# Kernel optimization log

Measured on AMD Instinct MI355X. Metric: run time of the kernel, lower is better.

The kernel has to match this reference:

```python
import jax, jax.numpy as jnp
import numpy as np

HID = 768
NUM_HEADS = 12
HEAD_DIM = HID // NUM_HEADS
MASK_VALUE = -1.0e9
EPS = 1.0e-4  # module's self.eps, also used as the diagonal fill constant


def setup_inputs() -> dict:
    key = jax.random.key(0)
    k1, k2, k3 = jax.random.split(key, 3)
    B, M = 16, 512
    ocr_features = jax.random.normal(k1, (B, M, HID), dtype=jnp.float32)
    # prior neighbor-attention from previous layer, probabilities in [0,1)
    prior = jax.random.uniform(k2, (B, 1, M, M), dtype=jnp.float32)
    Wq = jax.random.normal(k3, (HID, HID), dtype=jnp.float32) / np.sqrt(HID)
    bq = jnp.zeros((HID,), dtype=jnp.float32)
    ocr_features_mask = jnp.ones((B, M), dtype=jnp.int32)
    return {"ocr_features": ocr_features, "prior": prior, "Wq": Wq, "bq": bq,
            "ocr_features_mask": ocr_features_mask}


def reference(ocr_features, prior, Wq, bq, ocr_features_mask):
    B, M, _ = ocr_features.shape
    # Module uses q_linear for Q, K (and V, which is unused) -> Q == K.
    q = (ocr_features @ Wq + bq).reshape(B, M, NUM_HEADS, HEAD_DIM)
    q = q.transpose(0, 2, 1, 3)  # (B, H, M, D)
    # note: scaled by head_dim (not sqrt), as in the source
    scores = jnp.einsum('bhid,bhjd->bhij', q, q) / HEAD_DIM  # (B, H, M, M)

    dt = scores.dtype
    prev_word_mask = jnp.eye(M, k=1, dtype=dt)   # superdiagonal
    next_word_mask = jnp.eye(M, k=-1, dtype=dt)  # subdiagonal
    main_diag_mask = jnp.eye(M, dtype=dt)

    # neighbor mask: only prev/next word positions that are valid OCR tokens
    neibor_mask = ((prev_word_mask + next_word_mask)[None, :, :] > 0) & \
                  (ocr_features_mask[:, None, :] > 0)  # (B, M, M)
    scores = jnp.where(neibor_mask[:, None, :, :], scores, MASK_VALUE)
    neibor_attn = jax.nn.softmax(scores, axis=-1)
    # symmetrize: sqrt(a * a^T + eps)
    neibor_attn = jnp.sqrt(neibor_attn * jnp.swapaxes(neibor_attn, -1, -2) + EPS)
    neibor_attn = prior + (1.0 - prior) * neibor_attn

    # log-space cumulative product via triangular matmuls
    tri = jnp.triu(jnp.ones((M, M), dtype=dt))  # (M, M), incl. diagonal
    # keep only superdiagonal log-probs, cumulative-sum to the right via tri
    t = jnp.where(prev_word_mask > 0, jnp.log(neibor_attn + 1e-9), 0.0) @ tri
    g_attn = jnp.exp(jnp.einsum('ij,bhjk->bhik', tri, t))
    # zero out diagonal and lower triangle (tri - diag == 0 there)
    g_attn = jnp.where((tri - main_diag_mask) > 0, g_attn, 0.0)
    g_attn = g_attn + jnp.swapaxes(g_attn, -1, -2) + \
             jnp.where(main_diag_mask > 0, neibor_attn, EPS)
    return (g_attn, neibor_attn)
```

## Files before the change

### kernel.cpp

```cpp
#include <hip/hip_runtime.h>
#include <cstdint>
#include <cstddef>

#define B_   16
#define M_   512
#define HID_ 768
#define NH_  12
#define HD_  64

typedef short s16x8 __attribute__((ext_vector_type(8)));
typedef float f32x4 __attribute__((ext_vector_type(4)));
typedef unsigned short u16x8 __attribute__((ext_vector_type(8)));
typedef unsigned short u16x4 __attribute__((ext_vector_type(4)));

__device__ __forceinline__ unsigned short f2bf(float f) {
    unsigned int u = __builtin_bit_cast(unsigned int, f);
    u = u + 0x7FFFu + ((u >> 16) & 1u);
    return (unsigned short)(u >> 16);
}

__device__ __forceinline__ void gld_lds16(const void* g, void* lds) {
    __builtin_amdgcn_global_load_lds(
        (const __attribute__((address_space(1))) unsigned int*)g,
        (__attribute__((address_space(3))) unsigned int*)lds,
        16, 0, 0);
}

__launch_bounds__(256)
__global__ void convert_x(const float* __restrict__ X, unsigned short* __restrict__ Xb) {
    const size_t i = ((size_t)blockIdx.x * 256 + threadIdx.x) * 8;
    const float4 a = *(const float4*)(X + i);
    const float4 b = *(const float4*)(X + i + 4);
    u16x8 v = { f2bf(a.x), f2bf(a.y), f2bf(a.z), f2bf(a.w),
                f2bf(b.x), f2bf(b.y), f2bf(b.z), f2bf(b.w) };
    *(u16x8*)(Xb + i) = v;
}

__launch_bounds__(256)
__global__ void transpose_w(const float* __restrict__ W, unsigned short* __restrict__ Wt) {
    __shared__ float T[32][33];
    const int t  = threadIdx.x;
    const int n0 = blockIdx.x * 32;
    const int k0 = blockIdx.y * 32;
    #pragma unroll
    for (int p = 0; p < 4; ++p) {
        const int r = p * 8 + (t >> 5);
        const int c = t & 31;
        T[r][c] = W[(size_t)(k0 + r) * HID_ + n0 + c];
    }
    __syncthreads();
    const int nl = t >> 3;
    const int k4 = (t & 7) * 4;
    u16x4 v = { f2bf(T[k4 + 0][nl]), f2bf(T[k4 + 1][nl]),
                f2bf(T[k4 + 2][nl]), f2bf(T[k4 + 3][nl]) };
    *(u16x4*)(Wt + (size_t)(n0 + nl) * HID_ + k0 + k4) = v;
}

__launch_bounds__(256)
__global__ void gemm_qb(const unsigned short* __restrict__ Xb,
                        const unsigned short* __restrict__ Wt,
                        const float* __restrict__ bq, float* __restrict__ Q) {
    __shared__ unsigned short As[128 * 32];
    __shared__ unsigned short Bs[128 * 32];

    const int tid  = threadIdx.x;
    const int lane = tid & 63;
    const int wave = tid >> 6;
    const int wr   = (wave >> 1) * 64;
    const int wc   = (wave & 1) * 64;
    const int ln   = lane & 15;
    const int quad = lane >> 4;
    const int r0   = blockIdx.y * 128;
    const int n0   = blockIdx.x * 128;

    const int srow  = lane >> 2;
    const int skoff = (lane & 3) * 8;

    f32x4 acc[4][4] = {};

    for (int kt = 0; kt < HID_ / 32; ++kt) {
        const int k0 = kt * 32;
        #pragma unroll
        for (int c = wave * 2; c < wave * 2 + 2; ++c) {
            const unsigned short* ga = Xb + (size_t)(r0 + c * 16 + srow) * HID_ + k0 + skoff;
            gld_lds16(ga, (char*)As + c * 1024);
            const unsigned short* gb = Wt + (size_t)(n0 + c * 16 + srow) * HID_ + k0 + skoff;
            gld_lds16(gb, (char*)Bs + c * 1024);
        }
        __syncthreads();

        s16x8 af[4], bf[4];
        #pragma unroll
        for (int r = 0; r < 4; ++r)
            af[r] = *(const s16x8*)((const char*)As + (wr + r * 16 + ln) * 64 + quad * 16);
        #pragma unroll
        for (int c = 0; c < 4; ++c)
            bf[c] = *(const s16x8*)((const char*)Bs + (wc + c * 16 + ln) * 64 + quad * 16);
        #pragma unroll
        for (int r = 0; r < 4; ++r)
            #pragma unroll
            for (int c = 0; c < 4; ++c)
                acc[r][c] = __builtin_amdgcn_mfma_f32_16x16x32_bf16(af[r], bf[c], acc[r][c], 0, 0, 0);
        __syncthreads();
    }

    #pragma unroll
    for (int c = 0; c < 4; ++c) {
        const int col = n0 + wc + c * 16 + ln;
        const float bias = bq[col];
        #pragma unroll
        for (int r = 0; r < 4; ++r) {
            const int rowb = r0 + wr + r * 16 + quad * 4;
            #pragma unroll
            for (int e = 0; e < 4; ++e)
                Q[(size_t)(rowb + e) * HID_ + col] = acc[r][c][e] + bias;
        }
    }
}

__launch_bounds__(512)
__global__ void rowstats(const float* __restrict__ Q, const float* __restrict__ prior,
                         const int* __restrict__ mask,
                         float* __restrict__ na_super, float* __restrict__ na_sub,
                         float* __restrict__ Ssum) {
    const int bh = blockIdx.x;
    const int b  = bh / NH_;
    const int h  = bh - b * NH_;
    const int i  = threadIdx.x;

    __shared__ float sh_s[M_];
    __shared__ float sh_pp[M_];
    __shared__ float sc[2][M_];

    float s = 0.f;
    if (i < M_ - 1) {
        const float4* qa = (const float4*)(Q + (size_t)(b * M_ + i)     * HID_ + h * HD_);
        const float4* qb = (const float4*)(Q + (size_t)(b * M_ + i + 1) * HID_ + h * HD_);
        #pragma unroll
        for (int t = 0; t < 16; ++t) {
            float4 x = qa[t], y = qb[t];
            s += x.x * y.x + x.y * y.y + x.z * y.z + x.w * y.w;
        }
        s *= (1.f / 64.f);
    }
    sh_s[i] = s;
    __syncthreads();

    const bool vp = (i > 0)      && (mask[b * M_ + i - 1] > 0);
    const bool vn = (i < M_ - 1) && (mask[b * M_ + i + 1] > 0);
    const float sp = vp ? sh_s[i - 1] : -1e30f;
    const float sn = vn ? s : -1e30f;
    const float mx = fmaxf(sp, sn);
    const float ep = vp ? __expf(sp - mx) : 0.f;
    const float en = vn ? __expf(sn - mx) : 0.f;
    float den = ep + en;
    den = (den > 0.f) ? den : 1.f;
    const float pp = ep / den;
    const float pn = en / den;
    sh_pp[i] = pp;
    __syncthreads();

    float Lv = 0.f;
    if (i < M_ - 1) {
        const float  sym = sqrtf(pn * sh_pp[i + 1] + 1e-4f);
        const size_t pb  = (size_t)b * (M_ * M_);
        const float  prs = prior[pb + (size_t)i * M_ + (i + 1)];
        const float  prb = prior[pb + (size_t)(i + 1) * M_ + i];
        const float  nsup = prs + (1.f - prs) * sym;
        na_super[bh * M_ + i] = nsup;
        na_sub[bh * M_ + i]   = prb + (1.f - prb) * sym;
        Lv = logf(nsup + 1e-9f);
    }

    int pbuf = 0;
    sc[0][i] = Lv;
    __syncthreads();
    for (int off = 1; off < M_; off <<= 1) {
        float v = sc[pbuf][i] + ((i >= off) ? sc[pbuf][i - off] : 0.f);
        sc[pbuf ^ 1][i] = v;
        __syncthreads();
        pbuf ^= 1;
    }
    Ssum[bh * M_ + i] = (i > 0) ? sc[pbuf][i - 1] : 0.f;
}

__launch_bounds__(256)
__global__ void fill_out(const float* __restrict__ prior,
                         const float* __restrict__ na_super,
                         const float* __restrict__ na_sub,
                         const float* __restrict__ Ssum,
                         float* __restrict__ out) {
    const int tid = threadIdx.x;
    const int idx = blockIdx.x * 2 + (tid >> 7);
    const int h   = idx % NH_;
    const int tmp = idx / NH_;
    const int i   = tmp & (M_ - 1);
    const int b   = tmp >> 9;
    const int bh  = b * NH_ + h;
    const int j0  = (tid & 127) * 4;

    const float4 pr4 = *(const float4*)(prior + (size_t)b * (M_ * M_) + (size_t)i * M_ + j0);
    const float4 S4  = *(const float4*)(Ssum + bh * M_ + j0);
    const float  Si  = Ssum[bh * M_ + i];
    const float  nsup_i   = (i < M_ - 1) ? na_super[bh * M_ + i]     : 0.f;
    const float  nsub_im1 = (i > 0)      ? na_sub[bh * M_ + i - 1]   : 0.f;

    const float c0 = 0.00999999977f;

    const float pv[4] = {pr4.x, pr4.y, pr4.z, pr4.w};
    const float sv[4] = {S4.x, S4.y, S4.z, S4.w};
    float nav[4], ggv[4];
    #pragma unroll
    for (int e = 0; e < 4; ++e) {
        const int j = j0 + e;
        float na = fmaf(pv[e], 1.f - c0, c0);
        if (j == i - 1) na = nsub_im1;
        if (j == i + 1) na = nsup_i;
        const float d = sv[e] - Si;
        float g = __expf((j > i) ? d : -d) + 1e-4f;
        if (j == i) g = na;
        nav[e] = na;
        ggv[e] = g;
    }

    const size_t off  = ((size_t)(bh * M_ + i)) * M_ + j0;
    const size_t half = (size_t)B_ * NH_ * M_ * M_;
    f32x4 g4 = {ggv[0], ggv[1], ggv[2], ggv[3]};
    f32x4 n4 = {nav[0], nav[1], nav[2], nav[3]};
    __builtin_nontemporal_store(g4, (f32x4*)(out + off));
    __builtin_nontemporal_store(n4, (f32x4*)(out + half + off));
}

extern "C" void kernel_launch(void* const* d_in, const int* in_sizes, int n_in,
                              void* d_out, int out_size, void* d_ws, size_t ws_size,
                              hipStream_t stream) {
    const float* X     = (const float*)d_in[0];
    const float* prior = (const float*)d_in[1];
    const float* Wq    = (const float*)d_in[2];
    const float* bq    = (const float*)d_in[3];
    const int*   msk   = (const int*)  d_in[4];
    float* out = (float*)d_out;

    float* Q        = (float*)d_ws;
    float* na_super = Q + (size_t)B_ * M_ * HID_;
    float* na_sub   = na_super + (size_t)B_ * NH_ * M_;
    float* Ssum     = na_sub   + (size_t)B_ * NH_ * M_;
    unsigned short* Xb = (unsigned short*)(Ssum + (size_t)B_ * NH_ * M_);
    unsigned short* Wt = Xb + (size_t)B_ * M_ * HID_;

    convert_x<<<(B_ * M_ * HID_) / (256 * 8), 256, 0, stream>>>(X, Xb);
    transpose_w<<<dim3(HID_ / 32, HID_ / 32), 256, 0, stream>>>(Wq, Wt);

    dim3 gg(HID_ / 128, (B_ * M_) / 128);
    gemm_qb<<<gg, 256, 0, stream>>>(Xb, Wt, bq, Q);

    rowstats<<<B_ * NH_, M_, 0, stream>>>(Q, prior, msk, na_super, na_sub, Ssum);

    fill_out<<<(B_ * NH_ * M_) / 2, 256, 0, stream>>>(prior, na_super, na_sub, Ssum, out);
}
```

Before: 484.7 us.

## Merge prep kernels, use wave-shuffle scan, reuse prior row across heads

Fuses the bf16 conversion of X and the transpose of W into one launch. Replaces the shared-memory Hillis-Steele prefix scan in rowstats with a wave shuffle scan plus a per-wave base, cutting the number of barriers. fill_out now loops over all 12 heads per block so each prior row is loaded once rather than 12 times, and it switches from nontemporal stores to plain stores. The cost is fewer, longer-running fill blocks, and plain stores may pollute the cache on a write-bound kernel.

```diff
diff --git a/kernel.cpp b/kernel.cpp
--- a/kernel.cpp
+++ b/kernel.cpp
@@ -27,33 +27,35 @@
 }
 
 __launch_bounds__(256)
-__global__ void convert_x(const float* __restrict__ X, unsigned short* __restrict__ Xb) {
-    const size_t i = ((size_t)blockIdx.x * 256 + threadIdx.x) * 8;
-    const float4 a = *(const float4*)(X + i);
-    const float4 b = *(const float4*)(X + i + 4);
-    u16x8 v = { f2bf(a.x), f2bf(a.y), f2bf(a.z), f2bf(a.w),
-                f2bf(b.x), f2bf(b.y), f2bf(b.z), f2bf(b.w) };
-    *(u16x8*)(Xb + i) = v;
-}
-
-__launch_bounds__(256)
-__global__ void transpose_w(const float* __restrict__ W, unsigned short* __restrict__ Wt) {
+__global__ void prep(const float* __restrict__ X, const float* __restrict__ W,
+                     unsigned short* __restrict__ Xb, unsigned short* __restrict__ Wt) {
     __shared__ float T[32][33];
-    const int t  = threadIdx.x;
-    const int n0 = blockIdx.x * 32;
-    const int k0 = blockIdx.y * 32;
-    #pragma unroll
-    for (int p = 0; p < 4; ++p) {
-        const int r = p * 8 + (t >> 5);
-        const int c = t & 31;
-        T[r][c] = W[(size_t)(k0 + r) * HID_ + n0 + c];
-    }
-    __syncthreads();
-    const int nl = t >> 3;
-    const int k4 = (t & 7) * 4;
-    u16x4 v = { f2bf(T[k4 + 0][nl]), f2bf(T[k4 + 1][nl]),
-                f2bf(T[k4 + 2][nl]), f2bf(T[k4 + 3][nl]) };
-    *(u16x4*)(Wt + (size_t)(n0 + nl) * HID_ + k0 + k4) = v;
+    const int blk = blockIdx.x;
+    const int t   = threadIdx.x;
+    if (blk < 3072) {
+        const size_t i = ((size_t)blk * 256 + t) * 8;
+        const float4 a = *(const float4*)(X + i);
+        const float4 b = *(const float4*)(X + i + 4);
+        u16x8 v = { f2bf(a.x), f2bf(a.y), f2bf(a.z), f2bf(a.w),
+                    f2bf(b.x), f2bf(b.y), f2bf(b.z), f2bf(b.w) };
+        *(u16x8*)(Xb + i) = v;
+    } else {
+        const int tb = blk - 3072;
+        const int n0 = (tb % 24) * 32;
+        const int k0 = (tb / 24) * 32;
+        #pragma unroll
+        for (int p = 0; p < 4; ++p) {
+            const int r = p * 8 + (t >> 5);
+            const int c = t & 31;
+            T[r][c] = W[(size_t)(k0 + r) * HID_ + n0 + c];
+        }
+        __syncthreads();
+        const int nl = t >> 3;
+        const int k4 = (t & 7) * 4;
+        u16x4 v = { f2bf(T[k4 + 0][nl]), f2bf(T[k4 + 1][nl]),
+                    f2bf(T[k4 + 2][nl]), f2bf(T[k4 + 3][nl]) };
+        *(u16x4*)(Wt + (size_t)(n0 + nl) * HID_ + k0 + k4) = v;
+    }
 }
 
 __launch_bounds__(256)
@@ -127,10 +129,12 @@
     const int b  = bh / NH_;
     const int h  = bh - b * NH_;
     const int i  = threadIdx.x;
+    const int lane = i & 63;
+    const int wid  = i >> 6;
 
     __shared__ float sh_s[M_];
     __shared__ float sh_pp[M_];
-    __shared__ float sc[2][M_];
+    __shared__ float wsum[8];
 
     float s = 0.f;
     if (i < M_ - 1) {
@@ -172,16 +176,17 @@
         Lv = logf(nsup + 1e-9f);
     }
 
-    int pbuf = 0;
-    sc[0][i] = Lv;
+    float v = Lv;
+    #pragma unroll
+    for (int off = 1; off < 64; off <<= 1) {
+        float tt = __shfl_up(v, off, 64);
+        if (lane >= off) v += tt;
+    }
+    if (lane == 63) wsum[wid] = v;
     __syncthreads();
-    for (int off = 1; off < M_; off <<= 1) {
-        float v = sc[pbuf][i] + ((i >= off) ? sc[pbuf][i - off] : 0.f);
-        sc[pbuf ^ 1][i] = v;
-        __syncthreads();
-        pbuf ^= 1;
-    }
-    Ssum[bh * M_ + i] = (i > 0) ? sc[pbuf][i - 1] : 0.f;
+    float base = 0.f;
+    for (int w = 0; w < wid; ++w) base += wsum[w];
+    Ssum[bh * M_ + i] = v + base - Lv;
 }
 
 __launch_bounds__(256)
@@ -191,44 +196,43 @@
                          const float* __restrict__ Ssum,
                          float* __restrict__ out) {
     const int tid = threadIdx.x;
-    const int idx = blockIdx.x * 2 + (tid >> 7);
-    const int h   = idx % NH_;
-    const int tmp = idx / NH_;
-    const int i   = tmp & (M_ - 1);
-    const int b   = tmp >> 9;
-    const int bh  = b * NH_ + h;
+    const int bi  = blockIdx.x;
+    const int b   = bi >> 8;
+    const int i   = ((bi & 255) << 1) | (tid >> 7);
     const int j0  = (tid & 127) * 4;
 
     const float4 pr4 = *(const float4*)(prior + (size_t)b * (M_ * M_) + (size_t)i * M_ + j0);
-    const float4 S4  = *(const float4*)(Ssum + bh * M_ + j0);
-    const float  Si  = Ssum[bh * M_ + i];
-    const float  nsup_i   = (i < M_ - 1) ? na_super[bh * M_ + i]     : 0.f;
-    const float  nsub_im1 = (i > 0)      ? na_sub[bh * M_ + i - 1]   : 0.f;
-
+    const float pv[4] = {pr4.x, pr4.y, pr4.z, pr4.w};
     const float c0 = 0.00999999977f;
-
-    const float pv[4] = {pr4.x, pr4.y, pr4.z, pr4.w};
-    const float sv[4] = {S4.x, S4.y, S4.z, S4.w};
-    float nav[4], ggv[4];
-    #pragma unroll
-    for (int e = 0; e < 4; ++e) {
-        const int j = j0 + e;
-        float na = fmaf(pv[e], 1.f - c0, c0);
-        if (j == i - 1) na = nsub_im1;
-        if (j == i + 1) na = nsup_i;
-        const float d = sv[e] - Si;
-        float g = __expf((j > i) ? d : -d) + 1e-4f;
-        if (j == i) g = na;
-        nav[e] = na;
-        ggv[e] = g;
-    }
-
-    const size_t off  = ((size_t)(bh * M_ + i)) * M_ + j0;
     const size_t half = (size_t)B_ * NH_ * M_ * M_;
-    f32x4 g4 = {ggv[0], ggv[1], ggv[2], ggv[3]};
-    f32x4 n4 = {nav[0], nav[1], nav[2], nav[3]};
-    __builtin_nontemporal_store(g4, (f32x4*)(out + off));
-    __builtin_nontemporal_store(n4, (f32x4*)(out + half + off));
+
+    #pragma unroll 2
+    for (int h = 0; h < NH_; ++h) {
+        const int bh = b * NH_ + h;
+        const float4 S4 = *(const float4*)(Ssum + (size_t)bh * M_ + j0);
+        const float  Si = Ssum[bh * M_ + i];
+        const float  nsup_i   = (i < M_ - 1) ? na_super[bh * M_ + i]   : 0.f;
+        const float  nsub_im1 = (i > 0)      ? na_sub[bh * M_ + i - 1] : 0.f;
+        const float sv[4] = {S4.x, S4.y, S4.z, S4.w};
+
+        float nav[4], ggv[4];
+        #pragma unroll
+        for (int e = 0; e < 4; ++e) {
+            const int j = j0 + e;
+            float na = fmaf(pv[e], 1.f - c0, c0);
+            if (j == i - 1) na = nsub_im1;
+            if (j == i + 1) na = nsup_i;
+            const float d = sv[e] - Si;
+            float g = __expf((j > i) ? d : -d) + 1e-4f;
+            if (j == i) g = na;
+            nav[e] = na;
+            ggv[e] = g;
+        }
+
+        const size_t off = ((size_t)(bh * M_ + i)) * M_ + j0;
+        *(float4*)(out + off)        = make_float4(ggv[0], ggv[1], ggv[2], ggv[3]);
+        *(float4*)(out + half + off) = make_float4(nav[0], nav[1], nav[2], nav[3]);
+    }
 }
 
 extern "C" void kernel_launch(void* const* d_in, const int* in_sizes, int n_in,
@@ -248,13 +252,12 @@
     unsigned short* Xb = (unsigned short*)(Ssum + (size_t)B_ * NH_ * M_);
     unsigned short* Wt = Xb + (size_t)B_ * M_ * HID_;
 
-    convert_x<<<(B_ * M_ * HID_) / (256 * 8), 256, 0, stream>>>(X, Xb);
-    transpose_w<<<dim3(HID_ / 32, HID_ / 32), 256, 0, stream>>>(Wq, Wt);
+    prep<<<3072 + 576, 256, 0, stream>>>(X, Wq, Xb, Wt);
 
     dim3 gg(HID_ / 128, (B_ * M_) / 128);
     gemm_qb<<<gg, 256, 0, stream>>>(Xb, Wt, bq, Q);
 
     rowstats<<<B_ * NH_, M_, 0, stream>>>(Q, prior, msk, na_super, na_sub, Ssum);
 
-    fill_out<<<(B_ * NH_ * M_) / 2, 256, 0, stream>>>(prior, na_super, na_sub, Ssum, out);
-}
+    fill_out<<<B_ * (M_ / 2), 256, 0, stream>>>(prior, na_super, na_sub, Ssum, out);
+}
```

Measured after the change: 467.1 us. 1.04x faster.
